# Kernel optimization log

Hardware: AMD Instinct MI355X
Metric: run time of the kernel (lower is better)

## Reference

```python
import jax, jax.numpy as jnp
import numpy as np

N = 30000   # nodes
E = 480000  # edges (avg degree 16)
D = 256     # feat_dim == dim
H = 8       # heads
C = 32      # out channels per head (D // H, concat=True)
NEG = 0.2   # leaky-relu negative slope (args.alpha)
L = 2       # num_layers
NENC = 2 * L  # two GATv2 encoders (source/target direction) per layer


def setup_inputs() -> dict:
    key = jax.random.key(0)
    ks = jax.random.split(key, 10)
    s = jax.random.normal(ks[0], (N, D), dtype=jnp.float32)
    t = jax.random.normal(ks[1], (N, D), dtype=jnp.float32)
    edge_index = jax.random.randint(ks[2], (2, E), 0, N, dtype=jnp.int32)
    scale = 0.05
    Wl = jax.random.normal(ks[3], (NENC, D, H * C), dtype=jnp.float32) * scale
    bl = jnp.zeros((NENC, H * C), dtype=jnp.float32)
    Wr = jax.random.normal(ks[4], (NENC, D, H * C), dtype=jnp.float32) * scale
    br = jnp.zeros((NENC, H * C), dtype=jnp.float32)
    att = jax.random.normal(ks[5], (NENC, H, C), dtype=jnp.float32) * scale
    bias = jnp.zeros((NENC, H * C), dtype=jnp.float32)
    return {"s": s, "t": t, "Wl": Wl, "bl": bl, "Wr": Wr, "br": br,
            "att": att, "bias": bias, "edge_index": edge_index}


def _gatv2(x_src, x_dst, src, dst, Wl, bl, Wr, br, att, bias):
    """PyG GATv2Conv on bipartite input ((x_src, x_dst), edge_index).
    Messages flow src->dst, softmax-normalized over incoming edges of dst."""
    hl = (x_src @ Wl + bl).reshape(N, H, C)  # lin_l(source)
    hr = (x_dst @ Wr + br).reshape(N, H, C)  # lin_r(target)
    xe = hl[src] + hr[dst]                    # [E,H,C]
    e = jnp.where(xe > 0, xe, NEG * xe)       # leaky_relu
    logits = jnp.einsum('ehc,hc->eh', e, att)  # [E,H]
    m = jax.ops.segment_max(logits, dst, num_segments=N)
    m = jnp.where(jnp.isfinite(m), m, jnp.zeros_like(m))  # empty segments
    p = jnp.exp(logits - m[dst])
    denom = jax.ops.segment_sum(p, dst, num_segments=N)
    alpha = p / (denom[dst] + 1e-16)          # scatter-softmax weights [E,H]
    out = jax.ops.segment_sum(alpha[:, :, None] * hl[src], dst, num_segments=N)
    return out.reshape(N, H * C) + bias       # concat heads + bias


def reference(s, t, Wl, bl, Wr, br, att, bias, edge_index):
    src, dst = edge_index[0], edge_index[1]
    x_s, x_t = s, t
    for l in range(L):
        i, j = 2 * l, 2 * l + 1
        # source_encoder((s, t), edges): aggregate s-messages at t-nodes
        sh = _gatv2(x_s, x_t, src, dst, Wl[i], bl[i], Wr[i], br[i], att[i], bias[i])
        # target_encoder((t, s), flipped edges)
        th = _gatv2(x_t, x_s, dst, src, Wl[j], bl[j], Wr[j], br[j], att[j], bias[j])
        if l < L - 1:  # last layer activation is identity
            sh = jax.nn.relu(sh)
            th = jax.nn.relu(th)
        x_s, x_t = sh, th
    return x_s, x_t
```

## Files before the change

### kernel.cpp

```cpp
#include <hip/hip_runtime.h>
#include <hip/hip_bf16.h>

#define NNODES 30000
#define NEDGES 480000
#define HC 256
#define NEG_SLOPE 0.2f
#define NPART 8
#define EPP 60000
#define PN (NPART * NNODES)
#define SCAN_CHUNK 1024
#define NCHUNK2 235
#define NCHUNKM 30
#define CPP 235
#define NFE 7680000

typedef _Float16 half8 __attribute__((ext_vector_type(8)));
typedef _Float16 h4v __attribute__((ext_vector_type(4)));
typedef _Float16 h2 __attribute__((ext_vector_type(2)));
typedef float floatx4 __attribute__((ext_vector_type(4)));


__global__ void prep_kernel(const float* __restrict__ Wl, const float* __restrict__ Wr,
                            _Float16* __restrict__ WtL, _Float16* __restrict__ WtR,
                            const int* __restrict__ ei, int* __restrict__ deg_dst,
                            int* __restrict__ deg_src) {
    __shared__ float sh[32][33];
    int b = blockIdx.x;
    if (b < 512) {
        int e = b >> 6;
        int r0 = ((b >> 3) & 7) * 32, c0 = (b & 7) * 32;
        const float* W = (e < 4) ? Wl + (size_t)e * 65536 : Wr + (size_t)(e - 4) * 65536;
        _Float16* Wt = (e < 4) ? WtL + (size_t)e * 65536 : WtR + (size_t)(e - 4) * 65536;
        int x = threadIdx.x & 31, y = threadIdx.x >> 5;
#pragma unroll
        for (int j = 0; j < 4; j++) {
            int r = y + j * 8;
            sh[r][x] = W[(size_t)(r0 + r) * 256 + c0 + x];
        }
        __syncthreads();
#pragma unroll
        for (int j = 0; j < 4; j++) {
            int nn = y + j * 8;
            Wt[(size_t)(c0 + nn) * 256 + r0 + x] = (_Float16)sh[x][nn];
        }
    } else {
        b -= 512;
        int p = b & 7, c = b >> 3;
        int idx = c * 256 + threadIdx.x;
        if (idx >= EPP) return;
        int e = p * EPP + idx;
        int s = ei[e];
        int d = ei[NEDGES + e];
        atomicAdd(&deg_dst[p * NNODES + d], 1);
        atomicAdd(&deg_src[p * NNODES + s], 1);
    }
}

__global__ void mdeg_kernel(const int* __restrict__ deg_dst, const int* __restrict__ deg_src,
                            int* __restrict__ mdeg_dst, int* __restrict__ mdeg_src) {
    const int* deg = blockIdx.y ? deg_src : deg_dst;
    int* mdeg = blockIdx.y ? mdeg_src : mdeg_dst;
    int n = blockIdx.x * blockDim.x + threadIdx.x;
    if (n >= NNODES) return;
    int s = 0;
#pragma unroll
    for (int p = 0; p < NPART; p++) s += deg[p * NNODES + n];
    mdeg[n] = s;
}


__global__ void scanA_kernel(const int* __restrict__ deg_dst, const int* __restrict__ deg_src,
                             const int* __restrict__ mdeg_dst, const int* __restrict__ mdeg_src,
                             int* __restrict__ cur_dst, int* __restrict__ cur_src,
                             int* __restrict__ mrp_dst, int* __restrict__ mrp_src,
                             int* __restrict__ bsum) {
    __shared__ int sh[SCAN_CHUNK];
    const int y = blockIdx.y;
    const int nelem = (y < 2) ? PN : NNODES;
    if (blockIdx.x * SCAN_CHUNK >= nelem) return;
    const int* in = (y == 0) ? deg_dst : (y == 1) ? deg_src : (y == 2) ? mdeg_dst : mdeg_src;
    int t = threadIdx.x;
    int gid = blockIdx.x * SCAN_CHUNK + t;
    int v = (gid < nelem) ? in[gid] : 0;
    sh[t] = v;
    __syncthreads();
    for (int off = 1; off < SCAN_CHUNK; off <<= 1) {
        int u = (t >= off) ? sh[t - off] : 0;
        __syncthreads();
        sh[t] += u;
        __syncthreads();
    }
    if (gid < nelem) {
        if (y < 2) {
            int* cur = (y == 0) ? cur_dst : cur_src;
            cur[gid] = sh[t] - v;
        } else {
            int* mrp = (y == 2) ? mrp_dst : mrp_src;
            mrp[gid + 1] = sh[t];
        }
    }
    if (t == SCAN_CHUNK - 1) bsum[y * 256 + blockIdx.x] = sh[t];
}

__global__ void scan2_kernel(int* __restrict__ bsum) {
    int t = threadIdx.x;
    if (t < 4) {
        int cnt = (t < 2) ? NCHUNK2 : NCHUNKM;
        int run = 0;
        for (int i = 0; i < cnt; i++) {
            int v = bsum[t * 256 + i];
            bsum[t * 256 + i] = run;
            run += v;
        }
    }
}

__global__ void scanB_kernel(int* __restrict__ cur_dst, int* __restrict__ cur_src,
                             int* __restrict__ mrp_dst, int* __restrict__ mrp_src,
                             const int* __restrict__ bsum) {
    const int y = blockIdx.y;
    const int nelem = (y < 2) ? PN : NNODES;
    if (blockIdx.x * SCAN_CHUNK >= nelem) return;
    int t = threadIdx.x;
    int gid = blockIdx.x * SCAN_CHUNK + t;
    int base = bsum[y * 256 + blockIdx.x];
    if (gid < nelem) {
        if (y < 2) {
            ((y == 0) ? cur_dst : cur_src)[gid] += base;
        } else {
            ((y == 2) ? mrp_dst : mrp_src)[gid + 1] += base;
        }
    }
    if (gid == 0 && y >= 2) ((y == 2) ? mrp_dst : mrp_src)[0] = 0;
}

__global__ void fill_kernel(const int* __restrict__ ei, int* __restrict__ cur_dst,
                            int* __restrict__ cur_src, unsigned short* __restrict__ col_dst,
                            unsigned short* __restrict__ col_src) {
    int p = blockIdx.x & 7, c = blockIdx.x >> 3;
    int idx = c * 256 + threadIdx.x;
    if (idx >= EPP) return;
    int e = p * EPP + idx;
    int s = ei[e];
    int d = ei[NEDGES + e];
    int p0 = atomicAdd(&cur_dst[p * NNODES + d], 1);
    col_dst[p0] = (unsigned short)s;
    int p1 = atomicAdd(&cur_src[p * NNODES + s], 1);
    col_src[p1] = (unsigned short)d;
}

__global__ void merge_kernel(const int* __restrict__ deg_dst, const int* __restrict__ deg_src,
                             const int* __restrict__ cur_dst, const int* __restrict__ cur_src,
                             const int* __restrict__ mrp_dst, const int* __restrict__ mrp_src,
                             const unsigned short* __restrict__ col_dst,
                             const unsigned short* __restrict__ col_src,
                             unsigned short* __restrict__ mcol_dst,
                             unsigned short* __restrict__ mcol_src) {
    const int z = blockIdx.y;
    const int* deg = z ? deg_src : deg_dst;
    const int* cur = z ? cur_src : cur_dst;
    const int* mrp = z ? mrp_src : mrp_dst;
    const unsigned short* col = z ? col_src : col_dst;
    unsigned short* mcol = z ? mcol_src : mcol_dst;
    int n = blockIdx.x * blockDim.x + threadIdx.x;
    if (n >= NNODES) return;
    int w = mrp[n];
#pragma unroll
    for (int p = 0; p < NPART; p++) {
        int e = cur[p * NNODES + n];
        int d = deg[p * NNODES + n];
        for (int k = e - d; k < e; k++) mcol[w++] = col[k];
    }
}


__device__ inline half8 ldA8(const _Float16* p) { return *(const half8*)p; }
__device__ inline half8 ldA8(const float* p) {
    float4 a = *(const float4*)p;
    float4 b = *(const float4*)(p + 4);
    half8 r = {(_Float16)a.x, (_Float16)a.y, (_Float16)a.z, (_Float16)a.w,
               (_Float16)b.x, (_Float16)b.y, (_Float16)b.z, (_Float16)b.w};
    return r;
}

template <typename AT>
__global__ void __launch_bounds__(256)
gemm_f16(const AT* __restrict__ xs, const AT* __restrict__ xt,
         const _Float16* __restrict__ WtL, const _Float16* __restrict__ WtR,
         const float* __restrict__ bl, const float* __restrict__ br,
         _Float16* __restrict__ hbase, int e0) {
    const int y = blockIdx.y;
    const int e = e0 + (y >> 1);
    const AT* A = (y == 0 || y == 3) ? xs : xt;
    const bool left = (y & 1) == 0;
    const _Float16* Wt = (left ? WtL : WtR) + (size_t)e * 65536;
    const float* bvec = (left ? bl : br) + (size_t)e * HC;
    _Float16* C = hbase + (size_t)y * NFE;

    __shared__ __align__(16) _Float16 As[64 * 32];
    __shared__ __align__(16) _Float16 Bs[256 * 32];

    const int t = threadIdx.x;
    const int lane = t & 63, w = t >> 6;
    const int m0 = blockIdx.x * 64;
    const int rl = lane & 15, ch = lane >> 4;
    const int ar = t >> 2, ac = t & 3;

    floatx4 acc[4][4] = {};

    for (int k0 = 0; k0 < 256; k0 += 32) {
        half8 av = {};
        {
            int gr = m0 + ar;
            if (gr < NNODES) av = ldA8(A + (size_t)gr * 256 + k0 + ac * 8);
        }
        half8 bv[4];
#pragma unroll
        for (int j = 0; j < 4; j++) {
            int n = ar + j * 64;
            bv[j] = *(const half8*)(Wt + (size_t)n * 256 + k0 + ac * 8);
        }
        __syncthreads();
        *(half8*)(As + ar * 32 + (ac ^ ((ar >> 1) & 3)) * 8) = av;
#pragma unroll
        for (int j = 0; j < 4; j++) {
            int n = ar + j * 64;
            *(half8*)(Bs + n * 32 + (ac ^ ((n >> 1) & 3)) * 8) = bv[j];
        }
        __syncthreads();

        half8 a[4], b[4];
#pragma unroll
        for (int fm = 0; fm < 4; fm++) {
            int r = fm * 16 + rl;
            a[fm] = *(const half8*)(As + r * 32 + (ch ^ ((r >> 1) & 3)) * 8);
        }
#pragma unroll
        for (int fn = 0; fn < 4; fn++) {
            int n = w * 64 + fn * 16 + rl;
            b[fn] = *(const half8*)(Bs + n * 32 + (ch ^ ((n >> 1) & 3)) * 8);
        }
#pragma unroll
        for (int fm = 0; fm < 4; fm++)
#pragma unroll
            for (int fn = 0; fn < 4; fn++)
                acc[fm][fn] = __builtin_amdgcn_mfma_f32_16x16x32_f16(a[fm], b[fn], acc[fm][fn], 0, 0, 0);
    }

#pragma unroll
    for (int fn = 0; fn < 4; fn++) {
        int colb = w * 64 + fn * 16 + rl;
        float bb = bvec[colb];
#pragma unroll
        for (int fm = 0; fm < 4; fm++) {
#pragma unroll
            for (int j = 0; j < 4; j++) {
                int row = m0 + fm * 16 + ch * 4 + j;
                if (row < NNODES) C[(size_t)row * 256 + colb] = (_Float16)(acc[fm][fn][j] + bb);
            }
        }
    }
}


__device__ __forceinline__ void edge_body(half8 hv, half8 hrv, const float* att8,
                                          float* acc, float& denom, bool valid) {
    const h2 negv = {(_Float16)NEG_SLOPE, (_Float16)NEG_SLOPE};
    const h2* hvp = (const h2*)&hv;
    const h2* hrp = (const h2*)&hrv;
    float v = 0.f;
#pragma unroll
    for (int k = 0; k < 4; k++) {
        h2 x = hvp[k] + hrp[k];
        h2 lk = __builtin_elementwise_max(x, x * negv);
        v = fmaf((float)lk[0], att8[2 * k], v);
        v = fmaf((float)lk[1], att8[2 * k + 1], v);
    }
    v += __shfl_xor(v, 1);
    v += __shfl_xor(v, 2);
    float pe = __expf(v);
    if (!valid) pe = 0.f;
    denom += pe;
#pragma unroll
    for (int k = 0; k < 8; k++) acc[k] = fmaf((float)hv[k], pe, acc[k]);
}

__device__ inline void store8(float* p, const float* o) {
    *(float4*)p = make_float4(o[0], o[1], o[2], o[3]);
    *(float4*)(p + 4) = make_float4(o[4], o[5], o[6], o[7]);
}
__device__ inline void store8(_Float16* p, const float* o) {
    half8 h = {(_Float16)o[0], (_Float16)o[1], (_Float16)o[2], (_Float16)o[3],
               (_Float16)o[4], (_Float16)o[5], (_Float16)o[6], (_Float16)o[7]};
    *(half8*)p = h;
}

template <typename OT>
__global__ void __launch_bounds__(256)
agg_kernel(const _Float16* __restrict__ hbase,
           const int* __restrict__ mrp_dst, const unsigned short* __restrict__ mcol_dst,
           const int* __restrict__ mrp_src, const unsigned short* __restrict__ mcol_src,
           const float* __restrict__ att, const float* __restrict__ bias,
           OT* __restrict__ out0, OT* __restrict__ out1, int e0, int do_relu) {
    const int z = blockIdx.y;
    const _Float16* hl = hbase + (size_t)z * 2 * NFE;
    const _Float16* hr = hl + NFE;
    const int* mrp = z ? mrp_src : mrp_dst;
    const unsigned short* mcol = z ? mcol_src : mcol_dst;
    const float* attz = att + (size_t)(e0 + z) * HC;
    const float* biasz = bias + (size_t)(e0 + z) * HC;
    OT* out = z ? out1 : out0;

    int wave = threadIdx.x >> 6;
    int lane = threadIdx.x & 63;
    int n = blockIdx.x * 4 + wave;
    if (n >= NNODES) return;
    int h = lane >> 5;
    int cl = lane & 31;
    int c8 = cl << 3;

    half8 hrv = *(const half8*)(hr + (size_t)n * HC + c8);
    float att8[8];
    *(float4*)(att8) = *(const float4*)(attz + c8);
    *(float4*)(att8 + 4) = *(const float4*)(attz + c8 + 4);

    float acc[8] = {};
    float denom = 0.f;
    int beg = mrp[n], end = mrp[n + 1];

    int i = beg;
    for (; i + 4 <= end; i += 4) {
        int s0 = (int)mcol[i + h];
        int s1 = (int)mcol[i + 2 + h];
        half8 hv0 = *(const half8*)(hl + (size_t)s0 * HC + c8);
        half8 hv1 = *(const half8*)(hl + (size_t)s1 * HC + c8);
        edge_body(hv0, hrv, att8, acc, denom, true);
        edge_body(hv1, hrv, att8, acc, denom, true);
    }
    for (; i < end; i += 2) {
        int ei = i + h;
        bool valid = ei < end;
        int s0 = (int)mcol[valid ? ei : end - 1];
        half8 hv0 = *(const half8*)(hl + (size_t)s0 * HC + c8);
        edge_body(hv0, hrv, att8, acc, denom, valid);
    }

#pragma unroll
    for (int k = 0; k < 8; k++) acc[k] += __shfl_xor(acc[k], 32);
    denom += __shfl_xor(denom, 32);

    if (lane < 32) {
        float inv = 1.f / (denom + 1e-16f);
        float o[8];
        float b8[8];
        *(float4*)(b8) = *(const float4*)(biasz + c8);
        *(float4*)(b8 + 4) = *(const float4*)(biasz + c8 + 4);
#pragma unroll
        for (int k = 0; k < 8; k++) {
            o[k] = acc[k] * inv + b8[k];
            if (do_relu) o[k] = fmaxf(o[k], 0.f);
        }
        store8(out + (size_t)n * HC + c8, o);
    }
}


extern "C" void kernel_launch(void* const* d_in, const int* in_sizes, int n_in,
                              void* d_out, int out_size, void* d_ws, size_t ws_size,
                              hipStream_t stream) {
    const float* s = (const float*)d_in[0];
    const float* t = (const float*)d_in[1];
    const float* Wl = (const float*)d_in[2];
    const float* bl = (const float*)d_in[3];
    const float* Wr = (const float*)d_in[4];
    const float* br = (const float*)d_in[5];
    const float* att = (const float*)d_in[6];
    const float* bias = (const float*)d_in[7];
    const int* ei = (const int*)d_in[8];
    float* out = (float*)d_out;

    const size_t NF = (size_t)NFE;

    _Float16* os16 = (_Float16*)d_ws;
    _Float16* ot16 = os16 + NF;
    _Float16* hbase = ot16 + NF;
    _Float16* WtL = hbase + 4 * NF;
    _Float16* WtR = WtL + 4 * 65536;
    int* deg_dst = (int*)(WtR + 4 * 65536);
    int* deg_src = deg_dst + PN;
    int* cur_dst = deg_src + PN;
    int* cur_src = cur_dst + PN;
    int* mdeg_dst = cur_src + PN;
    int* mdeg_src = mdeg_dst + NNODES;
    int* mrp_dst = mdeg_src + NNODES;
    int* mrp_src = mrp_dst + (NNODES + 1);
    int* bsum = mrp_src + (NNODES + 1);
    unsigned short* col_dst = (unsigned short*)(bsum + 1024);
    unsigned short* col_src = col_dst + NEDGES;
    unsigned short* mcol_dst = col_src + NEDGES;
    unsigned short* mcol_src = mcol_dst + NEDGES;

    hipMemsetAsync(deg_dst, 0, 2 * PN * sizeof(int), stream);
    prep_kernel<<<512 + NPART * CPP, 256, 0, stream>>>(Wl, Wr, WtL, WtR, ei, deg_dst, deg_src);
    mdeg_kernel<<<dim3(118, 2), 256, 0, stream>>>(deg_dst, deg_src, mdeg_dst, mdeg_src);
    {
        dim3 g(NCHUNK2, 4);
        scanA_kernel<<<g, SCAN_CHUNK, 0, stream>>>(deg_dst, deg_src, mdeg_dst, mdeg_src,
                                                   cur_dst, cur_src, mrp_dst, mrp_src, bsum);
        scan2_kernel<<<1, 64, 0, stream>>>(bsum);
        scanB_kernel<<<g, SCAN_CHUNK, 0, stream>>>(cur_dst, cur_src, mrp_dst, mrp_src, bsum);
    }
    fill_kernel<<<NPART * CPP, 256, 0, stream>>>(ei, cur_dst, cur_src, col_dst, col_src);
    merge_kernel<<<dim3(118, 2), 256, 0, stream>>>(deg_dst, deg_src, cur_dst, cur_src,
                                                   mrp_dst, mrp_src, col_dst, col_src,
                                                   mcol_dst, mcol_src);

    dim3 ggemm((NNODES + 63) / 64, 4);
    dim3 gagg((NNODES + 3) / 4, 2);

    gemm_f16<float><<<ggemm, 256, 0, stream>>>(s, t, WtL, WtR, bl, br, hbase, 0);
    agg_kernel<_Float16><<<gagg, 256, 0, stream>>>(hbase, mrp_dst, mcol_dst, mrp_src, mcol_src,
                                                   att, bias, os16, ot16, 0, 1);
    gemm_f16<_Float16><<<ggemm, 256, 0, stream>>>(os16, ot16, WtL, WtR, bl, br, hbase, 2);
    agg_kernel<float><<<gagg, 256, 0, stream>>>(hbase, mrp_dst, mcol_dst, mrp_src, mcol_src,
                                                att, bias, out, out + NF, 2, 0);
}
```

Before: 393.9 us.

## Prefetch GEMM tiles, stage epilogue through LDS, unroll edge gather deeper

The GEMM now loads the next k-slice of A and W into registers while the current slice is multiplied, so global load latency overlaps the MFMA work. Its epilogue writes results into a padded shared-memory buffer and then stores full 16-byte rows to global, replacing scattered 2-byte stores. The edge aggregation loop gathers four neighbour rows per iteration instead of two and simplifies the tail handling to expose more memory parallelism. These changes cost more registers and extra synchronisations, which may reduce occupancy.

```diff
diff --git a/kernel.cpp b/kernel.cpp
--- a/kernel.cpp
+++ b/kernel.cpp
@@ -183,6 +183,8 @@
     return r;
 }
 
+#define EPI_STRIDE 264
+
 template <typename AT>
 __global__ void __launch_bounds__(256)
 gemm_f16(const AT* __restrict__ xs, const AT* __restrict__ xt,
@@ -197,8 +199,9 @@
     const float* bvec = (left ? bl : br) + (size_t)e * HC;
     _Float16* C = hbase + (size_t)y * NFE;
 
-    __shared__ __align__(16) _Float16 As[64 * 32];
-    __shared__ __align__(16) _Float16 Bs[256 * 32];
+    __shared__ __align__(16) _Float16 sh[10240];
+    _Float16* As = sh;
+    _Float16* Bs = sh + 2048;
 
     const int t = threadIdx.x;
     const int lane = t & 63, w = t >> 6;
@@ -208,18 +211,17 @@
 
     floatx4 acc[4][4] = {};
 
+    half8 av = {};
+    {
+        int gr = m0 + ar;
+        if (gr < NNODES) av = ldA8(A + (size_t)gr * 256 + ac * 8);
+    }
+    half8 bv[4];
+#pragma unroll
+    for (int j = 0; j < 4; j++)
+        bv[j] = *(const half8*)(Wt + (size_t)(ar + j * 64) * 256 + ac * 8);
+
     for (int k0 = 0; k0 < 256; k0 += 32) {
-        half8 av = {};
-        {
-            int gr = m0 + ar;
-            if (gr < NNODES) av = ldA8(A + (size_t)gr * 256 + k0 + ac * 8);
-        }
-        half8 bv[4];
-#pragma unroll
-        for (int j = 0; j < 4; j++) {
-            int n = ar + j * 64;
-            bv[j] = *(const half8*)(Wt + (size_t)n * 256 + k0 + ac * 8);
-        }
         __syncthreads();
         *(half8*)(As + ar * 32 + (ac ^ ((ar >> 1) & 3)) * 8) = av;
 #pragma unroll
@@ -229,6 +231,14 @@
         }
         __syncthreads();
 
+        if (k0 + 32 < 256) {
+            int gr = m0 + ar;
+            if (gr < NNODES) av = ldA8(A + (size_t)gr * 256 + (k0 + 32) + ac * 8);
+#pragma unroll
+            for (int j = 0; j < 4; j++)
+                bv[j] = *(const half8*)(Wt + (size_t)(ar + j * 64) * 256 + (k0 + 32) + ac * 8);
+        }
+
         half8 a[4], b[4];
 #pragma unroll
         for (int fm = 0; fm < 4; fm++) {
@@ -247,17 +257,35 @@
                 acc[fm][fn] = __builtin_amdgcn_mfma_f32_16x16x32_f16(a[fm], b[fn], acc[fm][fn], 0, 0, 0);
     }
 
-#pragma unroll
-    for (int fn = 0; fn < 4; fn++) {
-        int colb = w * 64 + fn * 16 + rl;
-        float bb = bvec[colb];
-#pragma unroll
-        for (int fm = 0; fm < 4; fm++) {
-#pragma unroll
-            for (int j = 0; j < 4; j++) {
-                int row = m0 + fm * 16 + ch * 4 + j;
-                if (row < NNODES) C[(size_t)row * 256 + colb] = (_Float16)(acc[fm][fn][j] + bb);
+    float bb[4];
+#pragma unroll
+    for (int fn = 0; fn < 4; fn++) bb[fn] = bvec[w * 64 + fn * 16 + rl];
+
+#pragma unroll
+    for (int hh = 0; hh < 2; hh++) {
+        __syncthreads();
+#pragma unroll
+        for (int f2 = 0; f2 < 2; f2++) {
+            int fm = hh * 2 + f2;
+#pragma unroll
+            for (int fn = 0; fn < 4; fn++) {
+                int colb = w * 64 + fn * 16 + rl;
+#pragma unroll
+                for (int j = 0; j < 4; j++) {
+                    int lr = f2 * 16 + ch * 4 + j;
+                    sh[lr * EPI_STRIDE + colb] = (_Float16)(acc[fm][fn][j] + bb[fn]);
+                }
             }
+        }
+        __syncthreads();
+        int lr = t >> 3;
+        int cseg = (t & 7) * 32;
+        int gr = m0 + hh * 32 + lr;
+        if (gr < NNODES) {
+#pragma unroll
+            for (int q = 0; q < 4; q++)
+                *(half8*)(C + (size_t)gr * 256 + cseg + q * 8) =
+                    *(const half8*)(sh + lr * EPI_STRIDE + cseg + q * 8);
         }
     }
 }
@@ -319,6 +347,7 @@
     int cl = lane & 31;
     int c8 = cl << 3;
 
+    const _Float16* hlc = hl + c8;
     half8 hrv = *(const half8*)(hr + (size_t)n * HC + c8);
     float att8[8];
     *(float4*)(att8) = *(const float4*)(attz + c8);
@@ -329,19 +358,29 @@
     int beg = mrp[n], end = mrp[n + 1];
 
     int i = beg;
-    for (; i + 4 <= end; i += 4) {
+    for (; i + 8 <= end; i += 8) {
         int s0 = (int)mcol[i + h];
         int s1 = (int)mcol[i + 2 + h];
-        half8 hv0 = *(const half8*)(hl + (size_t)s0 * HC + c8);
-        half8 hv1 = *(const half8*)(hl + (size_t)s1 * HC + c8);
+        int s2 = (int)mcol[i + 4 + h];
+        int s3 = (int)mcol[i + 6 + h];
+        half8 hv0 = *(const half8*)(hlc + ((size_t)s0 << 8));
+        half8 hv1 = *(const half8*)(hlc + ((size_t)s1 << 8));
+        half8 hv2 = *(const half8*)(hlc + ((size_t)s2 << 8));
+        half8 hv3 = *(const half8*)(hlc + ((size_t)s3 << 8));
         edge_body(hv0, hrv, att8, acc, denom, true);
         edge_body(hv1, hrv, att8, acc, denom, true);
-    }
-    for (; i < end; i += 2) {
-        int ei = i + h;
-        bool valid = ei < end;
-        int s0 = (int)mcol[valid ? ei : end - 1];
-        half8 hv0 = *(const half8*)(hl + (size_t)s0 * HC + c8);
+        edge_body(hv2, hrv, att8, acc, denom, true);
+        edge_body(hv3, hrv, att8, acc, denom, true);
+    }
+    for (; i + 2 <= end; i += 2) {
+        int s0 = (int)mcol[i + h];
+        half8 hv0 = *(const half8*)(hlc + ((size_t)s0 << 8));
+        edge_body(hv0, hrv, att8, acc, denom, true);
+    }
+    if (i < end) {
+        bool valid = (h == 0);
+        int s0 = (int)mcol[i];
+        half8 hv0 = *(const half8*)(hlc + ((size_t)s0 << 8));
         edge_body(hv0, hrv, att8, acc, denom, valid);
     }
 
```

After: 377.6 us. 4.1% less time.
